# Kernel tuning notes

Measured on AMD Instinct MI355X. Metric: run time of the kernel, lower is better.

The kernel has to match this reference:

```python
import jax, jax.numpy as jnp
import numpy as np

WS = 30       # window_size
ST = 15       # stride
TEMP = 0.1    # softmax temperature
FS = 30.0     # sampling rate (Hz)
LN_EPS = 1e-5


def setup_inputs() -> dict:
    key = jax.random.key(0)
    k = jax.random.split(key, 4)
    B, S = 4096, 9000
    D = 128
    x = jax.random.normal(k[0], (B, S), dtype=jnp.float32)
    W1 = jax.random.normal(k[1], (5, D // 2), dtype=jnp.float32) * (1.0 / np.sqrt(5))
    b1 = jnp.zeros((D // 2,), dtype=jnp.float32)
    W2 = jax.random.normal(k[2], (D // 2, D), dtype=jnp.float32) * (1.0 / np.sqrt(D // 2))
    b2 = jnp.zeros((D,), dtype=jnp.float32)
    gamma = jnp.ones((D,), dtype=jnp.float32)
    beta = jnp.zeros((D,), dtype=jnp.float32)
    return {"x": x, "W1": W1, "b1": b1, "W2": W2, "b2": b2, "gamma": gamma, "beta": beta}


def _prv_forward(x, W1, b1, W2, b2, gamma, beta):
    B, S = x.shape
    num_windows = (S - WS) // ST + 1
    starts = jnp.arange(num_windows) * ST                      # (NW,)
    idx = starts[:, None] + jnp.arange(WS)[None, :]            # (NW, WS)
    windows = x[:, idx]                                        # (B, NW, WS) gather
    w = jax.nn.softmax(windows / TEMP, axis=-1)                # (B, NW, WS)
    offsets = jnp.arange(WS, dtype=x.dtype)                    # (WS,)
    expected = jnp.sum(w * offsets, axis=-1)                   # (B, NW)
    peaks = expected + starts.astype(x.dtype)                  # absolute peak positions

    rr = (peaks[:, 1:] - peaks[:, :-1]) / FS                   # (B, N) RR intervals in sec
    mean_rr = jnp.mean(rr, axis=1, keepdims=True)
    diff_rr = rr[:, 1:] - rr[:, :-1]
    rmssd = jnp.sqrt(jnp.mean(diff_rr ** 2, axis=1, keepdims=True) + 1e-6)
    sdnn = jnp.std(rr, axis=1, keepdims=True, ddof=1)          # torch.std is unbiased

    n = rr.shape[1]
    n_fft = int(2 ** np.ceil(np.log2(n)))
    fft_rr = jnp.fft.rfft(rr, n=n_fft, axis=1)
    power = jnp.abs(fft_rr) ** 2                               # (B, n_fft//2+1)
    freqs = np.fft.rfftfreq(n_fft, d=1.0 / FS)                 # static, numpy
    lf_mask = jnp.asarray((freqs >= 0.04) & (freqs < 0.15))
    hf_mask = jnp.asarray((freqs >= 0.15) & (freqs <= 0.4))
    lf_power = jnp.sum(power * lf_mask, axis=1, keepdims=True)
    hf_power = jnp.sum(power * hf_mask, axis=1, keepdims=True)

    feats = jnp.concatenate([mean_rr, rmssd, sdnn, lf_power, hf_power], axis=1)  # (B, 5)
    h = jax.nn.relu(feats @ W1 + b1)
    h = h @ W2 + b2
    mu = jnp.mean(h, axis=-1, keepdims=True)
    var = jnp.var(h, axis=-1, keepdims=True)                   # biased, like torch LayerNorm
    return (h - mu) / jnp.sqrt(var + LN_EPS) * gamma + beta


def reference(x, W1, b1, W2, b2, gamma, beta):
    return _prv_forward(x, W1, b1, W2, b2, gamma, beta)
```

## Files before the change

### kernel.cpp

```cpp
#include <hip/hip_runtime.h>
#include <math.h>

#define NW 599
#define NRR 598

#define GLOAD16(gp, lp)                                                   \
  __builtin_amdgcn_global_load_lds(                                       \
      (const __attribute__((address_space(1))) void*)(gp),                \
      (__attribute__((address_space(3))) void*)(lp), 16, 0, 0)

__device__ inline float wave_allsum(float v) {
#pragma unroll
  for (int o = 32; o > 0; o >>= 1) v += __shfl_xor(v, o);
  return v;
}

__global__ __launch_bounds__(640) void peaks_kernel(
    const float* __restrict__ x, float* __restrict__ pk) {
  __shared__ float s[9760];
  const int row = blockIdx.x;
  const int tid = threadIdx.x;
  const int g = tid >> 6, lane = tid & 63;

  const float* __restrict__ src = x + (size_t)row * 9000 + 960 * g;
  float* dstf = s + g * 976;
  const int nfl = (g < 9) ? 976 : 360;

#pragma unroll
  for (int j = 0; j < 4; ++j) {
    const int f0 = j * 256 + lane * 4;
    if (f0 < nfl) GLOAD16(src + f0, dstf + j * 256);
  }
  asm volatile("s_waitcnt vmcnt(0)" ::: "memory");

  const int w = 64 * g + lane;
  if (w < NW) {
    const float* p = dstf + 15 * lane;
    float m = p[0];
#pragma unroll
    for (int j = 1; j < 30; ++j) m = fmaxf(m, p[j]);
    float se = 0.f, we = 0.f;
#pragma unroll
    for (int j = 0; j < 30; ++j) {
      float e = __expf((p[j] - m) * 10.0f);
      se += e;
      we += (float)j * e;
    }
    pk[(size_t)row * 600 + w] = we / se + 15.0f * (float)w;
  }
}

__global__ __launch_bounds__(512, 6) void feat_kernel(
    const float* __restrict__ pk, const float* __restrict__ W1,
    const float* __restrict__ b1, const float* __restrict__ W2,
    const float* __restrict__ b2, const float* __restrict__ gamma,
    const float* __restrict__ beta, float* __restrict__ out, int nrows) {
  const int tid = threadIdx.x;
  const int wid = tid >> 6, lane = tid & 63;
  const int row = blockIdx.x * 8 + wid;
  if (row >= nrows) return;

  const float* __restrict__ pkr = pk + (size_t)row * 600;
  const int n0 = lane * 10;
  const int cnt = max(0, min(NRR - n0, 10));

  const float inv30 = 1.0f / 30.0f;
  float p[11];
#pragma unroll
  for (int j = 0; j < 11; ++j) p[j] = (j <= cnt && cnt > 0) ? pkr[n0 + j] : 0.f;

  float rr[10];
#pragma unroll
  for (int j = 0; j < 10; ++j)
    rr[j] = (j < cnt) ? (p[j + 1] - p[j]) * inv30 : 0.f;

  float Srr = 0.f, Srr2 = 0.f, Sd2 = 0.f;
#pragma unroll
  for (int j = 0; j < 10; ++j) {
    Srr += rr[j];
    Srr2 = fmaf(rr[j], rr[j], Srr2);
    if (j < cnt - 1) {
      float d = rr[j + 1] - rr[j];
      Sd2 = fmaf(d, d, Sd2);
    }
  }
  float nxt0 = __shfl(rr[0], lane + 1);
  if (cnt > 0 && n0 + cnt - 1 <= NRR - 2) {
    float d = nxt0 - rr[cnt - 1];
    Sd2 = fmaf(d, d, Sd2);
  }

  const float c0 = 6.13592315154256491e-3f;
  float re[12], im[12];
#pragma unroll
  for (int kk = 0; kk < 12; ++kk) {
    const int k = kk + 2;
    float cb, sb, cs, ss;
    __sincosf((float)((k * n0) & 1023) * c0, &sb, &cb);
    __sincosf((float)k * c0, &ss, &cs);
    float r = 0.f, i2 = 0.f;
#pragma unroll
    for (int j = 0; j < 10; ++j) {
      if (j < cnt) {
        r = fmaf(rr[j], cb, r);
        i2 = fmaf(-rr[j], sb, i2);
      }
      float cb2 = cb * cs - sb * ss;
      sb = fmaf(sb, cs, cb * ss);
      cb = cb2;
    }
    re[kk] = r;
    im[kk] = i2;
  }

  Srr = wave_allsum(Srr);
  Srr2 = wave_allsum(Srr2);
  Sd2 = wave_allsum(Sd2);
  float lf = 0.f, hf = 0.f;
#pragma unroll
  for (int kk = 0; kk < 12; ++kk) {
    float r = wave_allsum(re[kk]);
    float i2 = wave_allsum(im[kk]);
    float pw = fmaf(r, r, i2 * i2);
    if (kk < 4) lf += pw; else hf += pw;
  }

  const float mean = Srr * (1.0f / (float)NRR);
  const float var =
      (Srr2 - (float)NRR * mean * mean) * (1.0f / (float)(NRR - 1));
  const float sdnn = sqrtf(fmaxf(var, 0.f));
  const float rmssd = sqrtf(Sd2 * (1.0f / (float)(NRR - 1)) + 1e-6f);

  float h1 = b1[lane];
  h1 = fmaf(mean, W1[lane], h1);
  h1 = fmaf(rmssd, W1[64 + lane], h1);
  h1 = fmaf(sdnn, W1[128 + lane], h1);
  h1 = fmaf(lf, W1[192 + lane], h1);
  h1 = fmaf(hf, W1[256 + lane], h1);
  h1 = fmaxf(h1, 0.f);

  float a0 = b2[lane], a1 = b2[64 + lane];
#pragma unroll 8
  for (int i = 0; i < 64; ++i) {
    float hv = __shfl(h1, i);
    a0 = fmaf(hv, W2[i * 128 + lane], a0);
    a1 = fmaf(hv, W2[i * 128 + 64 + lane], a1);
  }

  const float mu = wave_allsum(a0 + a1) * (1.0f / 128.0f);
  const float vv =
      wave_allsum((a0 - mu) * (a0 - mu) + (a1 - mu) * (a1 - mu)) *
      (1.0f / 128.0f);
  const float inv = rsqrtf(vv + 1e-5f);
  out[(size_t)row * 128 + lane] = (a0 - mu) * inv * gamma[lane] + beta[lane];
  out[(size_t)row * 128 + 64 + lane] =
      (a1 - mu) * inv * gamma[64 + lane] + beta[64 + lane];
}

extern "C" void kernel_launch(void* const* d_in, const int* in_sizes, int n_in,
                              void* d_out, int out_size, void* d_ws,
                              size_t ws_size, hipStream_t stream) {
  const float* x = (const float*)d_in[0];
  const float* W1 = (const float*)d_in[1];
  const float* b1 = (const float*)d_in[2];
  const float* W2 = (const float*)d_in[3];
  const float* b2 = (const float*)d_in[4];
  const float* gamma = (const float*)d_in[5];
  const float* beta = (const float*)d_in[6];
  float* out = (float*)d_out;

  const int B = in_sizes[0] / 9000;
  float* pk = (float*)d_ws;

  peaks_kernel<<<B, 640, 0, stream>>>(x, pk);
  feat_kernel<<<(B + 7) / 8, 512, 0, stream>>>(pk, W1, b1, W2, b2, gamma, beta,
                                               out, B);
}
```

Baseline: 47.86 us.

## Make peaks kernel persistent with per-wave double-buffered LDS prefetch

Replaces the one-block-per-row peaks kernel with a persistent grid of 256-thread blocks. Each wave independently processes 960-sample chunks in a grid-stride loop and double-buffers its global-to-LDS loads, so the next chunk is in flight while the softmax on the current one runs. The aim is to hide memory latency and cut block launch and scheduling overhead on this bandwidth-bound pass. In exchange it adds per-unit div/mod indexing, clamped tail loads, and a fixed grid size that may limit occupancy.

```diff
diff --git a/kernel.cpp b/kernel.cpp
--- a/kernel.cpp
+++ b/kernel.cpp
@@ -15,38 +15,74 @@
   return v;
 }
 
-__global__ __launch_bounds__(640) void peaks_kernel(
-    const float* __restrict__ x, float* __restrict__ pk) {
-  __shared__ float s[9760];
-  const int row = blockIdx.x;
+__global__ __launch_bounds__(256) void peaks_kernel(
+    const float* __restrict__ x, float* __restrict__ pk, int units,
+    int stride) {
+  __shared__ float s[4 * 2 * 976];
   const int tid = threadIdx.x;
-  const int g = tid >> 6, lane = tid & 63;
-
-  const float* __restrict__ src = x + (size_t)row * 9000 + 960 * g;
-  float* dstf = s + g * 976;
-  const int nfl = (g < 9) ? 976 : 360;
-
-#pragma unroll
-  for (int j = 0; j < 4; ++j) {
-    const int f0 = j * 256 + lane * 4;
-    if (f0 < nfl) GLOAD16(src + f0, dstf + j * 256);
-  }
-  asm volatile("s_waitcnt vmcnt(0)" ::: "memory");
-
-  const int w = 64 * g + lane;
-  if (w < NW) {
-    const float* p = dstf + 15 * lane;
-    float m = p[0];
-#pragma unroll
-    for (int j = 1; j < 30; ++j) m = fmaxf(m, p[j]);
-    float se = 0.f, we = 0.f;
-#pragma unroll
-    for (int j = 0; j < 30; ++j) {
-      float e = __expf((p[j] - m) * 10.0f);
-      se += e;
-      we += (float)j * e;
-    }
-    pk[(size_t)row * 600 + w] = we / se + 15.0f * (float)w;
+  const int wl = tid >> 6, lane = tid & 63;
+
+  float* bufA = s + wl * 1952;
+  float* bufB = bufA + 976;
+
+  int t = blockIdx.x * 4 + wl;
+  if (t >= units) return;
+
+  {
+    const unsigned tu = (unsigned)t;
+    const unsigned row = tu / 10u, g = tu % 10u;
+    const int nfl = (g < 9u) ? 976 : 360;
+    const float* src = x + (size_t)row * 9000 + 960 * g;
+#pragma unroll
+    for (int j = 0; j < 4; ++j) {
+      const int f0 = j * 256 + lane * 4;
+      const int f0c = min(f0, nfl - 4);
+      GLOAD16(src + f0c, bufA + j * 256);
+    }
+  }
+
+  for (; t < units; t += stride) {
+    const int tn = t + stride;
+    const bool pre = tn < units;
+    if (pre) {
+      const unsigned tu = (unsigned)tn;
+      const unsigned row = tu / 10u, g = tu % 10u;
+      const int nfl = (g < 9u) ? 976 : 360;
+      const float* src = x + (size_t)row * 9000 + 960 * g;
+#pragma unroll
+      for (int j = 0; j < 4; ++j) {
+        const int f0 = j * 256 + lane * 4;
+        const int f0c = min(f0, nfl - 4);
+        GLOAD16(src + f0c, bufB + j * 256);
+      }
+      asm volatile("s_waitcnt vmcnt(4)" ::: "memory");
+    } else {
+      asm volatile("s_waitcnt vmcnt(0)" ::: "memory");
+    }
+
+    {
+      const unsigned tu = (unsigned)t;
+      const unsigned row = tu / 10u, g = tu % 10u;
+      const int w = 64 * (int)g + lane;
+      if (w < NW) {
+        const float* p = bufA + 15 * lane;
+        float m = p[0];
+#pragma unroll
+        for (int j = 1; j < 30; ++j) m = fmaxf(m, p[j]);
+        float se = 0.f, we = 0.f;
+#pragma unroll
+        for (int j = 0; j < 30; ++j) {
+          float e = __expf((p[j] - m) * 10.0f);
+          se += e;
+          we += (float)j * e;
+        }
+        pk[(size_t)row * 600 + w] = we / se + 15.0f * (float)w;
+      }
+    }
+
+    float* tmp = bufA;
+    bufA = bufB;
+    bufB = tmp;
   }
 }
 
@@ -172,7 +208,12 @@
   const int B = in_sizes[0] / 9000;
   float* pk = (float*)d_ws;
 
-  peaks_kernel<<<B, 640, 0, stream>>>(x, pk);
+  const int units = B * 10;
+  int grid = 1280;
+  if (grid > (units + 3) / 4) grid = (units + 3) / 4;
+  const int stride = grid * 4;
+
+  peaks_kernel<<<grid, 256, 0, stream>>>(x, pk, units, stride);
   feat_kernel<<<(B + 7) / 8, 512, 0, stream>>>(pk, W1, b1, W2, b2, gamma, beta,
                                                out, B);
 }
```

Result: slower. 49.48 us (+3.4%).

## Stage peaks in LDS and interleave RR indices across lanes in feature kernel

Applied to the files above, without the earlier changes.

The feature kernel now copies each row's 600 peaks into shared memory with coalesced loads. Each lane then handles RR indices lane+64*j instead of a contiguous block of 10, which removes the cross-lane shuffle for the RMSSD term. The DFT twiddles are advanced by fixed per-step rotation constants (64 bins apart) across all 12 frequencies at once. Block size changes from 512 to 256 threads with 4 rows per block, and the peaks kernel uses an explicit FMA. The main cost targeted is strided, uncoalesced global reads of peaks. Trig work is now fused into a single loop, at the cost of more live registers (cb/sb/re/im arrays).

```diff
diff --git a/kernel.cpp b/kernel.cpp
--- a/kernel.cpp
+++ b/kernel.cpp
@@ -44,73 +44,80 @@
     for (int j = 0; j < 30; ++j) {
       float e = __expf((p[j] - m) * 10.0f);
       se += e;
-      we += (float)j * e;
+      we = fmaf((float)j, e, we);
     }
     pk[(size_t)row * 600 + w] = we / se + 15.0f * (float)w;
   }
 }
 
-__global__ __launch_bounds__(512, 6) void feat_kernel(
+__global__ __launch_bounds__(256, 4) void feat_kernel(
     const float* __restrict__ pk, const float* __restrict__ W1,
     const float* __restrict__ b1, const float* __restrict__ W2,
     const float* __restrict__ b2, const float* __restrict__ gamma,
     const float* __restrict__ beta, float* __restrict__ out, int nrows) {
+  __shared__ float s_pk[4][600];
   const int tid = threadIdx.x;
   const int wid = tid >> 6, lane = tid & 63;
-  const int row = blockIdx.x * 8 + wid;
+  const int row = blockIdx.x * 4 + wid;
   if (row >= nrows) return;
 
   const float* __restrict__ pkr = pk + (size_t)row * 600;
-  const int n0 = lane * 10;
-  const int cnt = max(0, min(NRR - n0, 10));
+  float* sp = s_pk[wid];
+#pragma unroll
+  for (int i = 0; i < 10; ++i) {
+    const int n = lane + 64 * i;
+    if (n < 600) sp[n] = pkr[n];
+  }
+
+  const float CS[12] = {0.70710678118654757f,  0.38268343236508984f,
+                        0.0f,                  -0.38268343236508984f,
+                        -0.70710678118654757f, -0.92387953251128674f,
+                        -1.0f,                 -0.92387953251128674f,
+                        -0.70710678118654757f, -0.38268343236508984f,
+                        0.0f,                  0.38268343236508984f};
+  const float SS[12] = {0.70710678118654757f,  0.92387953251128674f,
+                        1.0f,                  0.92387953251128674f,
+                        0.70710678118654757f,  0.38268343236508984f,
+                        0.0f,                  -0.38268343236508984f,
+                        -0.70710678118654757f, -0.92387953251128674f,
+                        -1.0f,                 -0.92387953251128674f};
+
+  const float c0 = 6.13592315154256491e-3f;
+  float cb[12], sb[12], re[12], im[12];
+#pragma unroll
+  for (int kk = 0; kk < 12; ++kk) {
+    const int k = kk + 2;
+    __sincosf((float)((k * lane) & 1023) * c0, &sb[kk], &cb[kk]);
+    re[kk] = 0.f;
+    im[kk] = 0.f;
+  }
 
   const float inv30 = 1.0f / 30.0f;
-  float p[11];
-#pragma unroll
-  for (int j = 0; j < 11; ++j) p[j] = (j <= cnt && cnt > 0) ? pkr[n0 + j] : 0.f;
-
-  float rr[10];
-#pragma unroll
-  for (int j = 0; j < 10; ++j)
-    rr[j] = (j < cnt) ? (p[j + 1] - p[j]) * inv30 : 0.f;
-
   float Srr = 0.f, Srr2 = 0.f, Sd2 = 0.f;
 #pragma unroll
   for (int j = 0; j < 10; ++j) {
-    Srr += rr[j];
-    Srr2 = fmaf(rr[j], rr[j], Srr2);
-    if (j < cnt - 1) {
-      float d = rr[j + 1] - rr[j];
-      Sd2 = fmaf(d, d, Sd2);
+    const int n = lane + 64 * j;
+    if (n < NRR) {
+      const float p0 = sp[n], p1 = sp[n + 1];
+      const float rv = (p1 - p0) * inv30;
+      Srr += rv;
+      Srr2 = fmaf(rv, rv, Srr2);
+      if (n < NRR - 1) {
+        const float d = (sp[n + 2] - 2.f * p1 + p0) * inv30;
+        Sd2 = fmaf(d, d, Sd2);
+      }
+#pragma unroll
+      for (int kk = 0; kk < 12; ++kk) {
+        re[kk] = fmaf(rv, cb[kk], re[kk]);
+        im[kk] = fmaf(-rv, sb[kk], im[kk]);
+      }
     }
-  }
-  float nxt0 = __shfl(rr[0], lane + 1);
-  if (cnt > 0 && n0 + cnt - 1 <= NRR - 2) {
-    float d = nxt0 - rr[cnt - 1];
-    Sd2 = fmaf(d, d, Sd2);
-  }
-
-  const float c0 = 6.13592315154256491e-3f;
-  float re[12], im[12];
 #pragma unroll
-  for (int kk = 0; kk < 12; ++kk) {
-    const int k = kk + 2;
-    float cb, sb, cs, ss;
-    __sincosf((float)((k * n0) & 1023) * c0, &sb, &cb);
-    __sincosf((float)k * c0, &ss, &cs);
-    float r = 0.f, i2 = 0.f;
-#pragma unroll
-    for (int j = 0; j < 10; ++j) {
-      if (j < cnt) {
-        r = fmaf(rr[j], cb, r);
-        i2 = fmaf(-rr[j], sb, i2);
-      }
-      float cb2 = cb * cs - sb * ss;
-      sb = fmaf(sb, cs, cb * ss);
-      cb = cb2;
+    for (int kk = 0; kk < 12; ++kk) {
+      const float c2 = cb[kk] * CS[kk] - sb[kk] * SS[kk];
+      sb[kk] = fmaf(sb[kk], CS[kk], cb[kk] * SS[kk]);
+      cb[kk] = c2;
     }
-    re[kk] = r;
-    im[kk] = i2;
   }
 
   Srr = wave_allsum(Srr);
@@ -119,9 +126,9 @@
   float lf = 0.f, hf = 0.f;
 #pragma unroll
   for (int kk = 0; kk < 12; ++kk) {
-    float r = wave_allsum(re[kk]);
-    float i2 = wave_allsum(im[kk]);
-    float pw = fmaf(r, r, i2 * i2);
+    const float r = wave_allsum(re[kk]);
+    const float i2 = wave_allsum(im[kk]);
+    const float pw = fmaf(r, r, i2 * i2);
     if (kk < 4) lf += pw; else hf += pw;
   }
 
@@ -142,7 +149,7 @@
   float a0 = b2[lane], a1 = b2[64 + lane];
 #pragma unroll 8
   for (int i = 0; i < 64; ++i) {
-    float hv = __shfl(h1, i);
+    const float hv = __shfl(h1, i);
     a0 = fmaf(hv, W2[i * 128 + lane], a0);
     a1 = fmaf(hv, W2[i * 128 + 64 + lane], a1);
   }
@@ -173,6 +180,6 @@
   float* pk = (float*)d_ws;
 
   peaks_kernel<<<B, 640, 0, stream>>>(x, pk);
-  feat_kernel<<<(B + 7) / 8, 512, 0, stream>>>(pk, W1, b1, W2, b2, gamma, beta,
+  feat_kernel<<<(B + 3) / 4, 256, 0, stream>>>(pk, W1, b1, W2, b2, gamma, beta,
                                                out, B);
 }
```

Result: faster. 46.88 us (-2.0%).
